# Optimization experiments

Measured on AMD Instinct MI355X. Metric: run time of the kernel, lower is better.

Reference implementation:

```python
import jax, jax.numpy as jnp
import numpy as np

NPOINT, RADIUS, SIGMA, K = 1024, 0.1, 0.05, 32
KDE_K = 128  # N_points default of kernel_density_estimation_ball


def setup_inputs() -> dict:
    key = jax.random.key(0)
    ks = jax.random.split(key, 9)
    B, N, C = 4, 4096, 16

    def glorot(k, shape):
        fan_in, fan_out = shape
        return jax.random.normal(k, shape, jnp.float32) * jnp.sqrt(2.0 / (fan_in + fan_out))

    return {
        'xyz': jax.random.uniform(ks[0], (B, N, 3), jnp.float32),      # unit cube
        'feature': jax.random.normal(ks[1], (B, N, C), jnp.float32),
        'w_mlp0': glorot(ks[2], (3 + C, 128)),
        'w_mlp1': glorot(ks[3], (128, 128)),
        'w_mlp2': glorot(ks[4], (128, 256)),
        'w_wn': glorot(ks[5], (3, 32)),
        'w_nl0': glorot(ks[6], (1, 16)),
        'w_nl1': glorot(ks[7], (16, 1)),
        'w_np': glorot(ks[8], (32, 256)),
    }


def _pdist2(a, b):
    # squared pairwise distances [B, M, N]
    return (jnp.sum(a * a, -1)[:, :, None] + jnp.sum(b * b, -1)[:, None, :]
            - 2.0 * jnp.einsum('bmd,bnd->bmn', a, b))


def _fps(xyz, npoint):
    # farthest point sampling, seeded at index 0 (matches CUDA op semantics)
    B, N, _ = xyz.shape

    def step(carry, _):
        min_d, last = carry
        p = jnp.take_along_axis(xyz, last[:, None, None], axis=1)  # [B,1,3]
        d = jnp.sum((xyz - p) ** 2, -1)                            # [B,N]
        min_d = jnp.minimum(min_d, d)
        nxt = jnp.argmax(min_d, axis=1).astype(jnp.int32)
        return (min_d, nxt), nxt

    init = (jnp.full((B, N), jnp.inf, xyz.dtype), jnp.zeros((B,), jnp.int32))
    _, rest = jax.lax.scan(step, init, None, length=npoint - 1)
    return jnp.concatenate([jnp.zeros((B, 1), jnp.int32), rest.T], axis=1)  # [B,npoint]


def _ball_query(xyz, radius, k):
    # first-k-in-index-order neighbors with d2 < r^2, padded with first hit
    B, N, _ = xyz.shape
    d2 = _pdist2(xyz, xyz)
    in_ball = d2 < radius * radius                 # self always included
    j = jnp.arange(N, dtype=jnp.int32)
    keys = jnp.where(in_ball, j, j + N)            # in-ball indices sort first
    _, idx = jax.lax.top_k(-keys, k)               # k smallest keys -> positions j
    cnt = jnp.minimum(jnp.sum(in_ball, axis=-1), k)            # [B,N]
    valid = jnp.arange(k) < cnt[..., None]
    idx = jnp.where(valid, idx, idx[..., :1])
    return idx, cnt


def _kde_ball(xyz, radius, sigma, kde_k):
    idx, cnt = _ball_query(xyz, radius, kde_k)     # [B,N,kde_k], [B,N]
    b_ix = jnp.arange(xyz.shape[0])[:, None, None]
    g = xyz[b_ix, idx] - xyz[:, :, None, :]        # [B,N,kde_k,3]
    R = jnp.sqrt(jnp.float32(sigma))
    quad = jnp.sum(jnp.square(g / R), axis=-1)     # [B,N,kde_k]
    mvn = jnp.exp(-0.5 * quad - 3.0 * jnp.log(R) - 1.5 * jnp.log(2.0 * 3.1415926))
    first = mvn[..., :1]
    total = jnp.sum(mvn, axis=-1, keepdims=True)
    cntf = cnt.astype(xyz.dtype)[..., None]
    total = total - first * (jnp.float32(kde_k) - cntf)  # remove padded duplicates
    return total / cntf                             # [B,N,1]


def _knn(k, src, q):
    d2 = _pdist2(q, src)                            # [B,P,N]
    _, idx = jax.lax.top_k(-d2, k)                  # ascending distance
    return idx


def _forward(xyz, feature, w_mlp0, w_mlp1, w_mlp2, w_wn, w_nl0, w_nl1, w_np):
    B = xyz.shape[0]
    conv = lambda x, w: jax.nn.relu(jnp.einsum('bpkc,cf->bpkf', x, w))  # bias-free 1x1 conv

    fps_idx = _fps(xyz, NPOINT)
    new_xyz = jnp.take_along_axis(xyz, fps_idx[..., None], axis=1)      # [B,P,3]

    knn_idx = _knn(K, xyz, new_xyz)                                      # [B,P,K]
    b_ix = jnp.arange(B)[:, None, None]
    grouped_xyz = xyz[b_ix, knn_idx] - new_xyz[:, :, None, :]            # [B,P,K,3]
    grouped_feature = jnp.concatenate([grouped_xyz, feature[b_ix, knn_idx]], axis=-1)

    inv_density = 1.0 / _kde_ball(xyz, RADIUS, SIGMA, KDE_K)             # [B,N,1]
    grouped_density = inv_density[b_ix, knn_idx]                          # [B,P,K,1]
    density_scale = grouped_density / jnp.max(grouped_density, axis=2, keepdims=True)

    h = conv(conv(conv(grouped_feature, w_mlp0), w_mlp1), w_mlp2)        # [B,P,K,256]
    weight = conv(grouped_xyz, w_wn)                                      # [B,P,K,32]
    density_scale = conv(conv(density_scale, w_nl0), w_nl1)               # [B,P,K,1]

    pts = h * density_scale
    pts = jnp.einsum('bpkc,bpkw->bpcw', pts, weight)                      # [B,P,256,32]
    # np_conv: 1x1 kernel with stride [1, mlp[-1]] + VALID -> only c=0 slice survives
    out = jax.nn.relu(jnp.einsum('bpw,wf->bpf', pts[:, :, 0, :], w_np))   # [B,P,256]
    return new_xyz, out


def reference(xyz, feature, w_mlp0, w_mlp1, w_mlp2, w_wn, w_nl0, w_nl1, w_np):
    return _forward(xyz, feature, w_mlp0, w_mlp1, w_mlp2, w_wn, w_nl0, w_nl1, w_np)
```

## Files before the change

kernel.cpp:

```cpp
#include <hip/hip_runtime.h>
#include <math.h>

#pragma clang fp contract(off)

typedef float v2f __attribute__((ext_vector_type(2)));

__global__ __launch_bounds__(256) void prep_kernel(
    const float* __restrict__ xyz, const float* __restrict__ w0,
    const float* __restrict__ w1, const float* __restrict__ w2,
    float* __restrict__ norms, float* __restrict__ W0T,
    float* __restrict__ W1T, float* __restrict__ W2c,
    unsigned* __restrict__ flag)
{
    int t = blockIdx.x * 256 + threadIdx.x;
    if (t == 0) *flag = 0u;
    if (t < 16384) {
        float x = xyz[t*3+0], y = xyz[t*3+1], z = xyz[t*3+2];
        norms[t] = (x*x + y*y) + z*z;
        int c = t >> 7, k = t & 127;
        W1T[c*128 + k] = w1[k*128 + c];
    }
    if (t < 2432) { int c = t / 19, i = t - c*19; W0T[t] = w0[i*128 + c]; }
    if (t < 128)  { W2c[t] = w2[t*256]; }
}

template<int CTRL>
__device__ __forceinline__ double dpp_f64(double v) {
    int lo = __double2loint(v), hi = __double2hiint(v);
    int plo = __builtin_amdgcn_update_dpp(lo, lo, CTRL, 0xF, 0xF, false);
    int phi = __builtin_amdgcn_update_dpp(hi, hi, CTRL, 0xF, 0xF, false);
    return __hiloint2double(phi, plo);
}
template<int CTRL>
__device__ __forceinline__ double max_f64_dpp(double k) {
    return fmax(dpp_f64<CTRL>(k), k);
}
#define KD(md2bits_f, ipi) __hiloint2double(__float_as_int(md2bits_f), (int)(ipi))

__global__ __launch_bounds__(512) void fps_kde_kernel(
    const float* __restrict__ xyz, const float* __restrict__ norms,
    float* __restrict__ new_xyz, float* __restrict__ invden,
    unsigned* __restrict__ flag)
{
    __shared__ float4 pts[4096];
    __shared__ float  nxb[3072];
    __shared__ __attribute__((aligned(16))) double swkd[2][4];
    int tid = threadIdx.x;

    if (blockIdx.x < 4) {
        int b = blockIdx.x;
        const float* Xb = xyz + b*12288;
        for (int t = tid; t < 4096; t += 512)
            pts[t] = make_float4(Xb[t*3+0], Xb[t*3+1], Xb[t*3+2], 0.0f);
        __syncthreads();
        if (tid < 256) {
            int lane = tid & 63, wave = tid >> 6;
            v2f Xp[8], Yp[8], Zp[8], md2[8];
            unsigned ip[16];
#pragma unroll
            for (int k = 0; k < 8; ++k) {
                float4 A = pts[(2*k)*256 + tid];
                float4 B = pts[(2*k+1)*256 + tid];
                Xp[k].x = A.x;  Xp[k].y = B.x;
                Yp[k].x = A.y;  Yp[k].y = B.y;
                Zp[k].x = A.z;  Zp[k].y = B.z;
                md2[k].x = INFINITY; md2[k].y = INFINITY;
                ip[2*k]   = ~((unsigned)((2*k)*256 + tid));
                ip[2*k+1] = ~((unsigned)((2*k+1)*256 + tid));
            }
            float cx = pts[0].x, cy = pts[0].y, cz = pts[0].z;
            if (tid == 0) { nxb[0] = cx; nxb[1] = cy; nxb[2] = cz; }
            int buf = 0;
            for (int it = 1; it < 1024; ++it) {
                v2f cx2, cy2, cz2;
                cx2.x = cx; cx2.y = cx;
                cy2.x = cy; cy2.y = cy;
                cz2.x = cz; cz2.y = cz;
#pragma unroll
                for (int k = 0; k < 8; ++k) {
                    v2f dx = Xp[k] - cx2, dy = Yp[k] - cy2, dz = Zp[k] - cz2;
                    v2f dd = (dx*dx + dy*dy) + dz*dz;
                    md2[k] = __builtin_elementwise_min(md2[k], dd);
                }
                double t0 = fmax(fmax(KD(md2[0].x,ip[0]),  KD(md2[0].y,ip[1])),
                                 fmax(KD(md2[1].x,ip[2]),  KD(md2[1].y,ip[3])));
                double t1 = fmax(fmax(KD(md2[2].x,ip[4]),  KD(md2[2].y,ip[5])),
                                 fmax(KD(md2[3].x,ip[6]),  KD(md2[3].y,ip[7])));
                double t2 = fmax(fmax(KD(md2[4].x,ip[8]),  KD(md2[4].y,ip[9])),
                                 fmax(KD(md2[5].x,ip[10]), KD(md2[5].y,ip[11])));
                double t3 = fmax(fmax(KD(md2[6].x,ip[12]), KD(md2[6].y,ip[13])),
                                 fmax(KD(md2[7].x,ip[14]), KD(md2[7].y,ip[15])));
                double key = fmax(fmax(t0, t1), fmax(t2, t3));
                key = max_f64_dpp<0xB1>(key);
                key = max_f64_dpp<0x4E>(key);
                key = max_f64_dpp<0x141>(key);
                key = max_f64_dpp<0x140>(key);
                key = max_f64_dpp<0x142>(key);
                key = max_f64_dpp<0x143>(key);
                if (lane == 63) swkd[buf][wave] = key;
                __syncthreads();
                double2 wab = *((const double2*)&swkd[buf][0]);
                double2 wcd = *((const double2*)&swkd[buf][2]);
                double kk = fmax(fmax(wab.x, wab.y), fmax(wcd.x, wcd.y));
                int fp = (int)(~((unsigned)__double2loint(kk)));
                float4 c = pts[fp];
                cx = c.x; cy = c.y; cz = c.z;
                if (tid == 0) { nxb[it*3+0] = cx; nxb[it*3+1] = cy; nxb[it*3+2] = cz; }
                buf ^= 1;
            }
        } else {
            for (int it = 1; it < 1024; ++it) __syncthreads();
        }
        __syncthreads();
        float* NX = new_xyz + b*3072;
        for (int t = tid; t < 3072; t += 512) NX[t] = nxb[t];
        if (tid == 0)
            __hip_atomic_fetch_add(flag, 1u, __ATOMIC_RELAXED,
                                   __HIP_MEMORY_SCOPE_AGENT);
    } else if (blockIdx.x < 2052) {
        int idx = blockIdx.x - 4;
        int b = idx >> 9;
        int wave = tid >> 6, lane = tid & 63;
        int i_local = ((idx & 511) << 3) + wave;
        const float* Xb = xyz + b*12288;
        const float* Nb = norms + b*4096;
        for (int t = tid; t < 4096; t += 512)
            pts[t] = make_float4(Xb[t*3+0], Xb[t*3+1], Xb[t*3+2], Nb[t]);
        __syncthreads();
        float4 c = pts[i_local];
        const float Rv    = sqrtf(0.05f);
        const float inv_s = 1.0f / (Rv*Rv);
        const float K1    = -3.0f*logf(Rv) - 1.5f*logf(2.0f*3.1415926f);
        float csum = 0.0f; int cnt = 0;
        for (int j = lane; j < 4096; j += 64) {
            float4 q = pts[j];
            float dot = (c.x*q.x + c.y*q.y) + c.z*q.z;
            float t2 = 2.0f * dot;
            float d2 = (c.w + q.w) - t2;
            if (d2 < 0.01f) {
                float gx = q.x - c.x, gy = q.y - c.y, gz = q.z - c.z;
                float dd = (gx*gx + gy*gy) + gz*gz;
                csum += expf(-0.5f * (dd * inv_s) + K1);
                cnt  += 1;
            }
        }
#pragma unroll
        for (int m = 1; m < 64; m <<= 1) {
            csum += __shfl_xor(csum, m, 64);
            cnt  += __shfl_xor(cnt,  m, 64);
        }
        if (lane == 0) {
            float den = csum / (float)cnt;
            invden[b*4096 + i_local] = 1.0f / den;
        }
    } else {
        float a = 1.0f + (float)tid * 1e-7f;
        const float bm = 1.000001f, cm = 0.999999f;
        while (__hip_atomic_load(flag, __ATOMIC_RELAXED,
                                 __HIP_MEMORY_SCOPE_AGENT) < 4u) {
            for (int i = 0; i < 512; ++i) a = fmaf(a, bm, cm);
        }
        asm volatile("" :: "v"(a));
    }
}

__global__ __launch_bounds__(256) void knn_kernel(
    const float* __restrict__ xyz, const float* __restrict__ norms,
    const float* __restrict__ new_xyz, int* __restrict__ knn_idx)
{
    __shared__ unsigned sd2[4*4096];
    __shared__ int sIdx[4*32];
    int wave = threadIdx.x >> 6, lane = threadIdx.x & 63;
    int qg = blockIdx.x*4 + wave;
    int b = qg >> 10;
    const float* Q = new_xyz + qg*3;
    float qx = Q[0], qy = Q[1], qz = Q[2];
    float nq = (qx*qx + qy*qy) + qz*qz;
    const float* Xb = xyz + b*12288;
    const float* Nb = norms + b*4096;
    unsigned* d2w = sd2 + wave*4096;
    for (int j = lane; j < 4096; j += 64) {
        float x = Xb[j*3+0], y = Xb[j*3+1], z = Xb[j*3+2];
        float dot = (qx*x + qy*y) + qz*z;
        float t2 = 2.0f*dot;
        float d = (nq + Nb[j]) - t2;
        unsigned u = __float_as_uint(d);
        unsigned m = ((unsigned)((int)u >> 31)) | 0x80000000u;
        d2w[j] = u ^ m;
    }
    for (int r = 0; r < 32; ++r) {
        double a0 = -INFINITY, a1 = -INFINITY, a2 = -INFINITY, a3 = -INFINITY;
#pragma unroll
        for (int t = 0; t < 16; ++t) {
            int jb = t*256 + lane*4;
            uint4 v = *((const uint4*)(d2w + jb));
            a0 = fmax(a0, __hiloint2double((int)v.x, jb));
            a1 = fmax(a1, __hiloint2double((int)v.y, jb+1));
            a2 = fmax(a2, __hiloint2double((int)v.z, jb+2));
            a3 = fmax(a3, __hiloint2double((int)v.w, jb+3));
        }
        double key = fmax(fmax(a0, a1), fmax(a2, a3));
        key = max_f64_dpp<0xB1>(key);
        key = max_f64_dpp<0x4E>(key);
        key = max_f64_dpp<0x141>(key);
        key = max_f64_dpp<0x140>(key);
        key = max_f64_dpp<0x142>(key);
        key = max_f64_dpp<0x143>(key);
        int jwin = __builtin_amdgcn_readlane(__double2loint(key), 63);
        if (lane == 0) { sIdx[wave*32 + r] = jwin; d2w[jwin] = 0xFFFFFFFFu; }
    }
    if (lane < 32) knn_idx[qg*32 + lane] = sIdx[wave*32 + lane];
}

__global__ __launch_bounds__(256, 2) void group_mlp_kernel(
    const float* __restrict__ xyz, const float* __restrict__ feat,
    const float* __restrict__ new_xyz, const int* __restrict__ knn_idx,
    const float* __restrict__ invden,
    const float* __restrict__ W0T, const float* __restrict__ W1T,
    const float* __restrict__ W2c, const float* __restrict__ wwn,
    const float* __restrict__ wnl0, const float* __restrict__ wnl1,
    float* __restrict__ ptsw)
{
    int row = blockIdx.x*256 + threadIdx.x;
    int k  = row & 31;
    int pg = row >> 5;
    int b  = row >> 15;
    int j  = knn_idx[row];
    const float* Xb = xyz + b*12288;
    const float* Q  = new_xyz + pg*3;
    float in[19];
    in[0] = Xb[j*3+0] - Q[0];
    in[1] = Xb[j*3+1] - Q[1];
    in[2] = Xb[j*3+2] - Q[2];
    const float4* F = (const float4*)(feat + (size_t)(b*4096 + j)*16);
    float4 f0 = F[0], f1 = F[1], f2 = F[2], f3 = F[3];
    in[3]=f0.x; in[4]=f0.y; in[5]=f0.z; in[6]=f0.w;
    in[7]=f1.x; in[8]=f1.y; in[9]=f1.z; in[10]=f1.w;
    in[11]=f2.x; in[12]=f2.y; in[13]=f2.z; in[14]=f2.w;
    in[15]=f3.x; in[16]=f3.y; in[17]=f3.z; in[18]=f3.w;

    float gd = invden[b*4096 + j];
    float mx = gd;
#pragma unroll
    for (int m = 1; m < 32; m <<= 1) mx = fmaxf(mx, __shfl_xor(mx, m, 64));
    float dsc = gd / mx;
    float sacc = 0.0f;
#pragma unroll
    for (int t = 0; t < 16; ++t)
        sacc = fmaf(fmaxf(dsc * wnl0[t], 0.0f), wnl1[t], sacc);
    float ds = fmaxf(sacc, 0.0f);

    float h1[128];
#pragma unroll
    for (int c = 0; c < 128; ++c) {
        const float* w = W0T + c*19;
        float a = in[0]*w[0];
#pragma unroll
        for (int i = 1; i < 19; ++i) a = fmaf(in[i], w[i], a);
        h1[c] = fmaxf(a, 0.0f);
    }
    float acc0 = 0.0f;
    for (int c2 = 0; c2 < 128; ++c2) {
        const float* w = W1T + c2*128;
        float a0 = 0.0f, a1 = 0.0f, a2 = 0.0f, a3 = 0.0f;
#pragma unroll
        for (int kk = 0; kk < 128; kk += 4) {
            a0 = fmaf(h1[kk+0], w[kk+0], a0);
            a1 = fmaf(h1[kk+1], w[kk+1], a1);
            a2 = fmaf(h1[kk+2], w[kk+2], a2);
            a3 = fmaf(h1[kk+3], w[kk+3], a3);
        }
        float a = (a0+a1) + (a2+a3);
        acc0 = fmaf(fmaxf(a, 0.0f), W2c[c2], acc0);
    }
    float h0 = fmaxf(acc0, 0.0f);
    float s = h0 * ds;

    float gx = in[0], gy = in[1], gz = in[2];
    float* pw = ptsw + pg*32;
#pragma unroll
    for (int w = 0; w < 32; ++w) {
        float a = gx * wwn[w];
        a = fmaf(gy, wwn[32+w], a);
        a = fmaf(gz, wwn[64+w], a);
        float part = s * fmaxf(a, 0.0f);
#pragma unroll
        for (int m = 1; m < 32; m <<= 1) part += __shfl_xor(part, m, 64);
        if (k == 0) pw[w] = part;
    }
}

__global__ __launch_bounds__(256) void final_kernel(
    const float* __restrict__ ptsw, const float* __restrict__ wnp,
    float* __restrict__ out)
{
    int pg = blockIdx.x;
    int f  = threadIdx.x;
    const float* pw = ptsw + pg*32;
    float a = 0.0f;
#pragma unroll
    for (int w = 0; w < 32; ++w) a = fmaf(pw[w], wnp[w*256+f], a);
    out[pg*256 + f] = fmaxf(a, 0.0f);
}

extern "C" void kernel_launch(void* const* d_in, const int* in_sizes, int n_in,
                              void* d_out, int out_size, void* d_ws, size_t ws_size,
                              hipStream_t stream) {
    const float* xyz  = (const float*)d_in[0];
    const float* feat = (const float*)d_in[1];
    const float* w0   = (const float*)d_in[2];
    const float* w1   = (const float*)d_in[3];
    const float* w2   = (const float*)d_in[4];
    const float* wwn  = (const float*)d_in[5];
    const float* wnl0 = (const float*)d_in[6];
    const float* wnl1 = (const float*)d_in[7];
    const float* wnp  = (const float*)d_in[8];

    float* out_all  = (float*)d_out;
    float* new_xyz  = out_all;
    float* out2     = out_all + 12288;

    char* ws = (char*)d_ws;
    float* norms  = (float*)(ws + 0);
    float* invden = (float*)(ws + 65536);
    int*   knn    = (int*)  (ws + 131072);
    float* ptsw   = (float*)(ws + 655360);
    float* W0T    = (float*)(ws + 1179648);
    float* W1T    = (float*)(ws + 1189376);
    float* W2c    = (float*)(ws + 1254912);
    unsigned* flag = (unsigned*)ptsw;

    prep_kernel<<<64, 256, 0, stream>>>(xyz, w0, w1, w2, norms, W0T, W1T, W2c,
                                        flag);
    fps_kde_kernel<<<2556, 512, 0, stream>>>(xyz, norms, new_xyz, invden, flag);
    knn_kernel<<<1024, 256, 0, stream>>>(xyz, norms, new_xyz, knn);
    group_mlp_kernel<<<512, 256, 0, stream>>>(xyz, feat, new_xyz, knn, invden,
                                              W0T, W1T, W2c, wwn, wnl0, wnl1, ptsw);
    final_kernel<<<4096, 256, 0, stream>>>(ptsw, wnp, out2);
}
```

Baseline: 824.9 us.

## Fuse final projection into group MLP, stage W1 in LDS, drop spin blocks

Removes the flag-driven busy-wait blocks from the FPS/KDE launch and adds an unused LDS pad to limit occupancy of that kernel. Stages the 128x128 W1 matrix in shared memory with float4 reads in the group MLP kernel, and fuses the final 32->256 projection into it via a small shared buffer, eliminating one launch and the intermediate global buffer. Risks include higher LDS pressure lowering occupancy and losing any clock or scheduling benefit the spin blocks provided.

```diff
diff --git a/kernel.cpp b/kernel.cpp
--- a/kernel.cpp
+++ b/kernel.cpp
@@ -9,11 +9,9 @@
     const float* __restrict__ xyz, const float* __restrict__ w0,
     const float* __restrict__ w1, const float* __restrict__ w2,
     float* __restrict__ norms, float* __restrict__ W0T,
-    float* __restrict__ W1T, float* __restrict__ W2c,
-    unsigned* __restrict__ flag)
+    float* __restrict__ W1T, float* __restrict__ W2c)
 {
     int t = blockIdx.x * 256 + threadIdx.x;
-    if (t == 0) *flag = 0u;
     if (t < 16384) {
         float x = xyz[t*3+0], y = xyz[t*3+1], z = xyz[t*3+2];
         norms[t] = (x*x + y*y) + z*z;
@@ -39,13 +37,14 @@
 
 __global__ __launch_bounds__(512) void fps_kde_kernel(
     const float* __restrict__ xyz, const float* __restrict__ norms,
-    float* __restrict__ new_xyz, float* __restrict__ invden,
-    unsigned* __restrict__ flag)
+    float* __restrict__ new_xyz, float* __restrict__ invden)
 {
     __shared__ float4 pts[4096];
     __shared__ float  nxb[3072];
     __shared__ __attribute__((aligned(16))) double swkd[2][4];
+    __shared__ float lds_pad[1024];
     int tid = threadIdx.x;
+    if (tid == 0x7fffffff) lds_pad[0] = 0.0f;
 
     if (blockIdx.x < 4) {
         int b = blockIdx.x;
@@ -114,10 +113,7 @@
         __syncthreads();
         float* NX = new_xyz + b*3072;
         for (int t = tid; t < 3072; t += 512) NX[t] = nxb[t];
-        if (tid == 0)
-            __hip_atomic_fetch_add(flag, 1u, __ATOMIC_RELAXED,
-                                   __HIP_MEMORY_SCOPE_AGENT);
-    } else if (blockIdx.x < 2052) {
+    } else {
         int idx = blockIdx.x - 4;
         int b = idx >> 9;
         int wave = tid >> 6, lane = tid & 63;
@@ -153,14 +149,6 @@
             float den = csum / (float)cnt;
             invden[b*4096 + i_local] = 1.0f / den;
         }
-    } else {
-        float a = 1.0f + (float)tid * 1e-7f;
-        const float bm = 1.000001f, cm = 0.999999f;
-        while (__hip_atomic_load(flag, __ATOMIC_RELAXED,
-                                 __HIP_MEMORY_SCOPE_AGENT) < 4u) {
-            for (int i = 0; i < 512; ++i) a = fmaf(a, bm, cm);
-        }
-        asm volatile("" :: "v"(a));
     }
 }
 
@@ -219,8 +207,18 @@
     const float* __restrict__ W0T, const float* __restrict__ W1T,
     const float* __restrict__ W2c, const float* __restrict__ wwn,
     const float* __restrict__ wnl0, const float* __restrict__ wnl1,
-    float* __restrict__ ptsw)
+    const float* __restrict__ wnp, float* __restrict__ out)
 {
+    __shared__ float sW1[16384];
+    __shared__ float sPW[8][33];
+    {
+        const float4* g4 = (const float4*)W1T;
+        float4* s4 = (float4*)sW1;
+#pragma unroll
+        for (int i = 0; i < 16; ++i)
+            s4[i*256 + threadIdx.x] = g4[i*256 + threadIdx.x];
+    }
+
     int row = blockIdx.x*256 + threadIdx.x;
     int k  = row & 31;
     int pg = row >> 5;
@@ -259,16 +257,19 @@
         for (int i = 1; i < 19; ++i) a = fmaf(in[i], w[i], a);
         h1[c] = fmaxf(a, 0.0f);
     }
+    __syncthreads();
+
     float acc0 = 0.0f;
     for (int c2 = 0; c2 < 128; ++c2) {
-        const float* w = W1T + c2*128;
+        const float4* w4 = (const float4*)(sW1 + c2*128);
         float a0 = 0.0f, a1 = 0.0f, a2 = 0.0f, a3 = 0.0f;
 #pragma unroll
-        for (int kk = 0; kk < 128; kk += 4) {
-            a0 = fmaf(h1[kk+0], w[kk+0], a0);
-            a1 = fmaf(h1[kk+1], w[kk+1], a1);
-            a2 = fmaf(h1[kk+2], w[kk+2], a2);
-            a3 = fmaf(h1[kk+3], w[kk+3], a3);
+        for (int kk = 0; kk < 32; ++kk) {
+            float4 wv = w4[kk];
+            a0 = fmaf(h1[4*kk+0], wv.x, a0);
+            a1 = fmaf(h1[4*kk+1], wv.y, a1);
+            a2 = fmaf(h1[4*kk+2], wv.z, a2);
+            a3 = fmaf(h1[4*kk+3], wv.w, a3);
         }
         float a = (a0+a1) + (a2+a3);
         acc0 = fmaf(fmaxf(a, 0.0f), W2c[c2], acc0);
@@ -277,7 +278,7 @@
     float s = h0 * ds;
 
     float gx = in[0], gy = in[1], gz = in[2];
-    float* pw = ptsw + pg*32;
+    int l = threadIdx.x >> 5;
 #pragma unroll
     for (int w = 0; w < 32; ++w) {
         float a = gx * wwn[w];
@@ -286,21 +287,22 @@
         float part = s * fmaxf(a, 0.0f);
 #pragma unroll
         for (int m = 1; m < 32; m <<= 1) part += __shfl_xor(part, m, 64);
-        if (k == 0) pw[w] = part;
-    }
-}
-
-__global__ __launch_bounds__(256) void final_kernel(
-    const float* __restrict__ ptsw, const float* __restrict__ wnp,
-    float* __restrict__ out)
-{
-    int pg = blockIdx.x;
-    int f  = threadIdx.x;
-    const float* pw = ptsw + pg*32;
-    float a = 0.0f;
-#pragma unroll
-    for (int w = 0; w < 32; ++w) a = fmaf(pw[w], wnp[w*256+f], a);
-    out[pg*256 + f] = fmaxf(a, 0.0f);
+        if (k == 0) sPW[l][w] = part;
+    }
+    __syncthreads();
+
+    int f = threadIdx.x;
+    float wc[32];
+#pragma unroll
+    for (int w = 0; w < 32; ++w) wc[w] = wnp[w*256 + f];
+    int pg0 = blockIdx.x * 8;
+#pragma unroll
+    for (int r = 0; r < 8; ++r) {
+        float a = 0.0f;
+#pragma unroll
+        for (int w = 0; w < 32; ++w) a = fmaf(sPW[r][w], wc[w], a);
+        out[(pg0 + r)*256 + f] = fmaxf(a, 0.0f);
+    }
 }
 
 extern "C" void kernel_launch(void* const* d_in, const int* in_sizes, int n_in,
@@ -324,17 +326,14 @@
     float* norms  = (float*)(ws + 0);
     float* invden = (float*)(ws + 65536);
     int*   knn    = (int*)  (ws + 131072);
-    float* ptsw   = (float*)(ws + 655360);
-    float* W0T    = (float*)(ws + 1179648);
-    float* W1T    = (float*)(ws + 1189376);
-    float* W2c    = (float*)(ws + 1254912);
-    unsigned* flag = (unsigned*)ptsw;
-
-    prep_kernel<<<64, 256, 0, stream>>>(xyz, w0, w1, w2, norms, W0T, W1T, W2c,
-                                        flag);
-    fps_kde_kernel<<<2556, 512, 0, stream>>>(xyz, norms, new_xyz, invden, flag);
+    float* W0T    = (float*)(ws + 655360);
+    float* W1T    = (float*)(ws + 665088);
+    float* W2c    = (float*)(ws + 730624);
+
+    prep_kernel<<<64, 256, 0, stream>>>(xyz, w0, w1, w2, norms, W0T, W1T, W2c);
+    fps_kde_kernel<<<2052, 512, 0, stream>>>(xyz, norms, new_xyz, invden);
     knn_kernel<<<1024, 256, 0, stream>>>(xyz, norms, new_xyz, knn);
     group_mlp_kernel<<<512, 256, 0, stream>>>(xyz, feat, new_xyz, knn, invden,
-                                              W0T, W1T, W2c, wwn, wnl0, wnl1, ptsw);
-    final_kernel<<<4096, 256, 0, stream>>>(ptsw, wnp, out2);
-}
+                                              W0T, W1T, W2c, wwn, wnl0, wnl1,
+                                              wnp, out2);
+}
```

New measurement: 795.2 us. -3.6%, faster.
